# Kernel tuning notes

Hardware: AMD Instinct MI355X
Metric: run time of the kernel (lower is better)

Reference implementation:

```python
import jax, jax.numpy as jnp
import numpy as np
import math

EPS = 1e-5
GROUPS = 8


def setup_inputs() -> dict:
    key = jax.random.key(0)
    ks = jax.random.split(key, 4)
    b, c, h, w = 4, 256, 64, 64
    x = jax.random.normal(ks[0], (b, c, h, w), dtype=jnp.float32)
    norm_w = jnp.ones((c,), dtype=jnp.float32)
    norm_b = jnp.zeros((c,), dtype=jnp.float32)
    qkv_w = jax.random.normal(ks[1], (3 * c, c), dtype=jnp.float32) * (1.0 / math.sqrt(c))
    qkv_b = jnp.zeros((3 * c,), dtype=jnp.float32)
    proj_w = jax.random.normal(ks[2], (c, c), dtype=jnp.float32) * (1.0 / math.sqrt(c))
    proj_b = jnp.zeros((c,), dtype=jnp.float32)
    return {"x": x, "norm_w": norm_w, "norm_b": norm_b, "qkv_w": qkv_w,
            "qkv_b": qkv_b, "proj_w": proj_w, "proj_b": proj_b}


def group_norm(x, weight, bias):
    b, c, h, w = x.shape
    xg = x.reshape(b, GROUPS, c // GROUPS, h, w)
    mean = xg.mean(axis=(2, 3, 4), keepdims=True)
    var = xg.var(axis=(2, 3, 4), keepdims=True)
    xg = (xg - mean) * jax.lax.rsqrt(var + EPS)
    xn = xg.reshape(b, c, h, w)
    return xn * weight[None, :, None, None] + bias[None, :, None, None]


def reference(x, norm_w, norm_b, qkv_w, qkv_b, proj_w, proj_b):
    b, c, h, w = x.shape
    n = h * w
    xn = group_norm(x, norm_w, norm_b)
    # 1x1 conv == per-pixel linear: tokens [b, n, c]
    tokens = xn.reshape(b, c, n).transpose(0, 2, 1)
    qkv = jnp.einsum('bnc,oc->bno', tokens, qkv_w) + qkv_b  # [b, n, 3c]
    q, k, v = jnp.split(qkv, 3, axis=-1)
    scale = 1.0 / math.sqrt(c)
    attn = jnp.einsum('bqc,bkc->bqk', q, k) * scale  # [b, n, n]
    attn = jax.nn.softmax(attn, axis=-1)
    out = jnp.einsum('bqk,bkc->bqc', attn, v)  # [b, n, c]
    out = jnp.einsum('bnc,oc->bno', out, proj_w) + proj_b
    out = out.transpose(0, 2, 1).reshape(b, c, h, w)
    return x + out
```

## Files before the change

### kernel.cpp

```cpp
#include <hip/hip_runtime.h>
#include <math.h>

typedef unsigned short u16;
typedef __bf16 bf16x8 __attribute__((ext_vector_type(8)));
typedef u16    u16x8  __attribute__((ext_vector_type(8)));
typedef float  f32x4  __attribute__((ext_vector_type(4)));
typedef float  f32x16 __attribute__((ext_vector_type(16)));

__device__ __forceinline__ float b2f(u16 u) {
    union { unsigned u; float f; } x; x.u = ((unsigned)u) << 16; return x.f;
}
__device__ __forceinline__ u16 f2b(float f) {
    union { float f; unsigned u; } x; x.f = f;
    unsigned r = x.u + 0x7FFFu + ((x.u >> 16) & 1u);
    return (u16)(r >> 16);
}
__device__ __forceinline__ f32x4 mfma16(bf16x8 a, bf16x8 b, f32x4 c) {
    return __builtin_amdgcn_mfma_f32_16x16x32_bf16(a, b, c, 0, 0, 0);
}
__device__ __forceinline__ f32x16 mfma32(bf16x8 a, bf16x8 b, f32x16 c) {
    return __builtin_amdgcn_mfma_f32_32x32x16_bf16(a, b, c, 0, 0, 0);
}
__device__ __forceinline__ void dma16(const void* g, void* l) {
    __builtin_amdgcn_global_load_lds((const __attribute__((address_space(1))) void*)g,
                                     (__attribute__((address_space(3))) void*)l, 16, 0, 0);
}
__device__ __forceinline__ int dtype_vote(const unsigned* w) {
    unsigned v = w[threadIdx.x & 63];
    unsigned e = ((v & 0xFFFFu) >> 7) & 0xFFu;
    unsigned long long m = __ballot(e >= 0x60u && e <= 0x8Fu);
    return (__popcll(m) >= 32) ? 0 : 1;
}

#define QSCALE 0.09016844f

__global__ __launch_bounds__(256) void k_cvtx(const void* __restrict__ src, u16* __restrict__ dst,
                                              int* __restrict__ flag) {
    const int f = dtype_vote((const unsigned*)src);
    if (blockIdx.x == 0 && threadIdx.x == 0) *flag = f;
    const int i = (blockIdx.x * 256 + threadIdx.x) * 4;
    if (f) {
        float4 v = *(const float4*)((const float*)src + i);
        unsigned lo = (unsigned)f2b(v.x) | ((unsigned)f2b(v.y) << 16);
        unsigned hi = (unsigned)f2b(v.z) | ((unsigned)f2b(v.w) << 16);
        *(uint2*)(dst + i) = make_uint2(lo, hi);
    } else {
        *(uint2*)(dst + i) = *(const uint2*)((const u16*)src + i);
    }
}

__global__ __launch_bounds__(256) void k_cvtp(const void* s0, const void* s1, const void* s2,
                                              const void* s3, const void* s4, const void* s5,
                                              u16* d0, u16* d1, u16* d2, u16* d3, u16* d4, u16* d5) {
    const int f = dtype_vote((const unsigned*)s2);
    const int i = blockIdx.x * 256 + threadIdx.x;
    const void* s; u16* d; int j;
    if      (i < 256)    { s = s0; d = d0; j = i; }
    else if (i < 512)    { s = s1; d = d1; j = i - 256; }
    else if (i < 197120) { s = s2; d = d2; j = i - 512; }
    else if (i < 197888) { s = s3; d = d3; j = i - 197120; }
    else if (i < 263424) { s = s4; d = d4; j = i - 197888; }
    else if (i < 263680) { s = s5; d = d5; j = i - 263424; }
    else return;
    if (f) d[j] = f2b(((const float*)s)[j]);
    else   d[j] = ((const u16*)s)[j];
}

__global__ __launch_bounds__(256) void k_stats(const u16* __restrict__ x, float* __restrict__ stats) {
    const int bg = blockIdx.x;
    const u16* p = x + (size_t)bg * 131072;
    float s = 0.f, ss = 0.f;
    for (int i = threadIdx.x; i < 16384; i += 256) {
        bf16x8 v = *(const bf16x8*)(p + i * 8);
#pragma unroll
        for (int j = 0; j < 8; j++) { float f = (float)v[j]; s += f; ss += f * f; }
    }
#pragma unroll
    for (int o = 1; o < 64; o <<= 1) { s += __shfl_xor(s, o, 64); ss += __shfl_xor(ss, o, 64); }
    __shared__ float rs[4], rss[4];
    const int wv = threadIdx.x >> 6;
    if ((threadIdx.x & 63) == 0) { rs[wv] = s; rss[wv] = ss; }
    __syncthreads();
    if (threadIdx.x == 0) {
        s = rs[0] + rs[1] + rs[2] + rs[3];
        ss = rss[0] + rss[1] + rss[2] + rss[3];
        float mean = s * (1.f / 131072.f);
        float var = fmaxf(ss * (1.f / 131072.f) - mean * mean, 0.f);
        stats[bg] = mean;
        stats[32 + bg] = rsqrtf(var + 1e-5f);
    }
}

__global__ __launch_bounds__(256) void k_tok(const u16* __restrict__ x, const u16* __restrict__ nw,
                                             const u16* __restrict__ nb, const float* __restrict__ stats,
                                             u16* __restrict__ tok) {
    const int b = blockIdx.z, c0 = blockIdx.y * 64, p0 = blockIdx.x * 64;
    __shared__ u16 t[64][72];
    const int cl = threadIdx.x >> 2, seg = threadIdx.x & 3;
    const int c = c0 + cl;
    const int g = c >> 5;
    const float mean = stats[b * 8 + g], rstd = stats[32 + b * 8 + g];
    const float scale = b2f(nw[c]) * rstd;
    const float shift = b2f(nb[c]) - mean * scale;
    const u16* xp = x + ((size_t)(b * 256 + c)) * 4096 + p0 + seg * 16;
#pragma unroll
    for (int h = 0; h < 2; h++) {
        bf16x8 v = *(const bf16x8*)(xp + h * 8);
#pragma unroll
        for (int j = 0; j < 8; j++)
            t[seg * 16 + h * 8 + j][cl] = f2b((float)v[j] * scale + shift);
    }
    __syncthreads();
    u16x8 o0, o1;
#pragma unroll
    for (int j = 0; j < 8; j++) { o0[j] = t[cl][seg * 16 + j]; o1[j] = t[cl][seg * 16 + 8 + j]; }
    u16* op = tok + ((size_t)(b * 4096 + p0 + cl)) * 256 + c0 + seg * 16;
    *(u16x8*)op = o0;
    *((u16x8*)op + 1) = o1;
}

__global__ __launch_bounds__(256) void k_qkv(const u16* __restrict__ A, const u16* __restrict__ W,
                                             const u16* __restrict__ bias,
                                             u16* __restrict__ Qo, u16* __restrict__ Ko, u16* __restrict__ Vt) {
    const int m0 = blockIdx.x * 128, n0 = blockIdx.y * 128;
    const int tid = threadIdx.x, w = tid >> 6, lane = tid & 63, l15 = lane & 15, l4 = lane >> 4;
    const int wm = w >> 1, wn = w & 1;
    __shared__ __attribute__((aligned(16))) u16 At[128 * 64];
    __shared__ __attribute__((aligned(16))) u16 Bt[128 * 64];
    f32x4 acc[4][4];
    const f32x4 z = {0.f, 0.f, 0.f, 0.f};
#pragma unroll
    for (int i = 0; i < 4; i++)
#pragma unroll
        for (int j = 0; j < 4; j++) acc[i][j] = z;

    for (int kt = 0; kt < 4; kt++) {
        const int k0 = kt * 64;
#pragma unroll
        for (int i = 0; i < 4; i++) {
            int v = tid + i * 256;
            int row = v >> 3, c8 = v & 7;
            int swz = (c8 ^ (row & 7)) << 3;
            *(u16x8*)(&At[row * 64 + swz]) = *(const u16x8*)(A + (size_t)(m0 + row) * 256 + k0 + c8 * 8);
            *(u16x8*)(&Bt[row * 64 + swz]) = *(const u16x8*)(W + (size_t)(n0 + row) * 256 + k0 + c8 * 8);
        }
        __syncthreads();
#pragma unroll
        for (int ks = 0; ks < 2; ks++) {
            const int sc = ((ks * 4 + l4) ^ (l15 & 7)) << 3;
            bf16x8 af[4], bfr[4];
#pragma unroll
            for (int i = 0; i < 4; i++) {
                af[i]  = *(const bf16x8*)(&At[(wm * 64 + i * 16 + l15) * 64 + sc]);
                bfr[i] = *(const bf16x8*)(&Bt[(wn * 64 + i * 16 + l15) * 64 + sc]);
            }
#pragma unroll
            for (int i = 0; i < 4; i++)
#pragma unroll
                for (int j = 0; j < 4; j++) acc[i][j] = mfma16(af[i], bfr[j], acc[i][j]);
        }
        __syncthreads();
    }
#pragma unroll
    for (int j = 0; j < 4; j++) {
        const int n = n0 + wn * 64 + j * 16 + l15;
        const float bia = b2f(bias[n]);
#pragma unroll
        for (int i = 0; i < 4; i++) {
#pragma unroll
            for (int r = 0; r < 4; r++) {
                const int m = m0 + wm * 64 + i * 16 + l4 * 4 + r;
                const float vv = acc[i][j][r] + bia;
                if (n < 256)       Qo[(size_t)m * 256 + n] = f2b(vv * QSCALE);
                else if (n < 512)  Ko[(size_t)m * 256 + (n - 256)] = f2b(vv);
                else {
                    const int bb = m >> 12;
                    int p = m & 4095;
                    int d = ((p >> 2) ^ (p >> 3)) & 1;
                    p ^= d * 12;
                    Vt[((size_t)bb * 256 + (n - 512)) * 4096 + p] = f2b(vv);
                }
            }
        }
    }
}

__global__ __launch_bounds__(256, 2) void k_attn(const u16* __restrict__ Q, const u16* __restrict__ K,
                                                 const u16* __restrict__ Vt,
                                                 u16* __restrict__ Up, float* __restrict__ ml) {
    const int qt = blockIdx.x, b = blockIdx.y, sp = blockIdx.z;
    const int tid = threadIdx.x, w = tid >> 6, lane = tid & 63;
    const int l31 = lane & 31, h = lane >> 5;
    const int qcol = qt * 128 + w * 32 + l31;

    __shared__ __attribute__((aligned(16))) char LB[65536];
    u16* KT = (u16*)LB;
    u16* VT = (u16*)(LB + 32768);

    bf16x8 aq[16];
    {
        const u16* qp = Q + ((size_t)(b * 4096 + qcol)) * 256 + h * 8;
#pragma unroll
        for (int kb = 0; kb < 16; kb++) aq[kb] = *(const bf16x8*)(qp + kb * 16);
    }
    f32x16 acc[8];
#pragma unroll
    for (int ct = 0; ct < 8; ct++)
#pragma unroll
        for (int r = 0; r < 16; r++) acc[ct][r] = 0.f;
    float m_i = -3e38f, l_i = 0.f;

    const char* Kg0 = (const char*)(K + (size_t)(b * 4096 + sp * 1024) * 256);
    const char* Vg0 = (const char*)(Vt + (size_t)b * 256 * 4096 + sp * 1024);
    const int wb = (tid & 192) * 8;

#define ISSUE(bi, kt)                                                                        \
    {                                                                                        \
        const char* Kg = Kg0 + (size_t)(kt) * 32 * 512;                                      \
        const char* Vg = Vg0 + (size_t)(kt) * 64;                                            \
        _Pragma("unroll")                                                                    \
        for (int i = 0; i < 4; i++) {                                                        \
            int q = i * 256 + tid;                                                           \
            int row = q >> 5, c = q & 31;                                                    \
            dma16(Kg + row * 512 + ((c ^ row) << 4), &KT[(bi) * 8192 + (i * 256) * 8 + wb]); \
        }                                                                                    \
        _Pragma("unroll")                                                                    \
        for (int i = 0; i < 4; i++) {                                                        \
            int q = i * 256 + tid;                                                           \
            int row = q >> 2, c = q & 3;                                                     \
            dma16(Vg + (size_t)row * 8192 + ((c ^ ((row >> 3) & 3)) << 4),                   \
                  &VT[(bi) * 8192 + (i * 256) * 8 + wb]);                                    \
        }                                                                                    \
    }

    ISSUE(0, 0)
    ISSUE(1, 1)

    for (int kt = 0; kt < 32; kt++) {
        const int cur = kt & 1;
        if (kt < 31) asm volatile("s_waitcnt vmcnt(8)" ::: "memory");
        else         asm volatile("s_waitcnt vmcnt(0)" ::: "memory");
        asm volatile("s_barrier" ::: "memory");

        const u16* KTc = &KT[cur * 8192];
        const u16* VTc = &VT[cur * 8192];

        f32x16 st;
#pragma unroll
        for (int r = 0; r < 16; r++) st[r] = 0.f;
#pragma unroll
        for (int kb = 0; kb < 16; kb++) {
            bf16x8 bk = *(const bf16x8*)(&KTc[l31 * 256 + (((kb * 2 + h) ^ l31) << 3)]);
            st = mfma32(bk, aq[kb], st);
        }

        float mx = st[0];
#pragma unroll
        for (int r = 1; r < 16; r++) mx = fmaxf(mx, st[r]);
        mx = fmaxf(mx, __shfl_xor(mx, 32, 64));
        if (__any(mx > m_i + 4.f)) {
            const float m_new = fmaxf(m_i, mx);
            const float al = __builtin_amdgcn_exp2f(m_i - m_new);
#pragma unroll
            for (int ct = 0; ct < 8; ct++)
#pragma unroll
                for (int r = 0; r < 16; r++) acc[ct][r] *= al;
            l_i *= al;
            m_i = m_new;
        }
        float sum = 0.f;
#pragma unroll
        for (int r = 0; r < 16; r++) {
            st[r] = __builtin_amdgcn_exp2f(st[r] - m_i);
            sum += st[r];
        }
        sum += __shfl_xor(sum, 32, 64);
        l_i += sum;

        union { u16x8 u; bf16x8 bv; } p0, p1;
#pragma unroll
        for (int e = 0; e < 8; e++) { p0.u[e] = f2b(st[e]); p1.u[e] = f2b(st[8 + e]); }

#pragma unroll
        for (int ct = 0; ct < 8; ct++) {
            bf16x8 av0 = *(const bf16x8*)(&VTc[(ct * 32 + l31) * 32 + ((h ^ (l31 >> 3)) << 3)]);
            acc[ct] = mfma32(av0, p0.bv, acc[ct]);
            bf16x8 av1 = *(const bf16x8*)(&VTc[(ct * 32 + l31) * 32 + (((2 + h) ^ (l31 >> 3)) << 3)]);
            acc[ct] = mfma32(av1, p1.bv, acc[ct]);
        }
        asm volatile("s_barrier" ::: "memory");
        if (kt + 2 < 32) ISSUE(cur, kt + 2)
    }
#undef ISSUE

    if (h == 0)
        ((float2*)ml)[(size_t)(sp * 4 + b) * 4096 + qcol] = make_float2(m_i, l_i);
    u16* Ot = (u16*)(LB + w * 16384);
#pragma unroll
    for (int ct = 0; ct < 8; ct++) {
#pragma unroll
        for (int r = 0; r < 16; r++) {
            const int c = ct * 32 + (r & 3) + 8 * (r >> 2) + 4 * h;
            Ot[l31 * 256 + (((c >> 3) ^ l31) << 3) + (c & 7)] = f2b(acc[ct][r]);
        }
    }
    u16* up = Up + ((size_t)(sp * 4 + b) * 4096 + qt * 128 + w * 32) * 256;
#pragma unroll
    for (int v = 0; v < 16; v++) {
        int idx = v * 64 + lane;
        int qrow = idx >> 5, c8 = idx & 31;
        u16x8 d = *(const u16x8*)(&Ot[qrow * 256 + ((c8 ^ qrow) << 3)]);
        *(u16x8*)(up + (size_t)qrow * 256 + c8 * 8) = d;
    }
}

__global__ __launch_bounds__(256) void k_ml(const float* __restrict__ ml, float4* __restrict__ W4q) {
    const int t = blockIdx.x * 256 + threadIdx.x;
    const int b = t >> 12, q = t & 4095;
    float m_s[4], l_s[4];
#pragma unroll
    for (int s = 0; s < 4; s++) {
        float2 v = ((const float2*)ml)[(size_t)(s * 4 + b) * 4096 + q];
        m_s[s] = v.x; l_s[s] = v.y;
    }
    float M = fmaxf(fmaxf(m_s[0], m_s[1]), fmaxf(m_s[2], m_s[3]));
    float L = 0.f, e[4];
#pragma unroll
    for (int s = 0; s < 4; s++) { e[s] = __builtin_amdgcn_exp2f(m_s[s] - M); L += l_s[s] * e[s]; }
    float inv = 1.f / fmaxf(L, 1e-30f);
    W4q[t] = make_float4(e[0] * inv, e[1] * inv, e[2] * inv, e[3] * inv);
}

__global__ __launch_bounds__(256) void k_proj(const u16* __restrict__ Up, const float4* __restrict__ W4q,
                                              const u16* __restrict__ W, const u16* __restrict__ bias,
                                              const u16* __restrict__ x, void* __restrict__ out,
                                              const int* __restrict__ flag) {
    const int f32out = *flag;
    const int m0 = blockIdx.x * 64;
    const int b = m0 >> 12, q0 = m0 & 4095;
    const int tid = threadIdx.x, w = tid >> 6, lane = tid & 63, l15 = lane & 15, l4 = lane >> 4;
    const int wm = w >> 1, wn = w & 1;
    __shared__ __attribute__((aligned(16))) char PL[40960];
    u16* At = (u16*)PL;
    u16* Bt = (u16*)(PL + 8192);
    u16* Ot = (u16*)PL;

    const int qa = tid >> 2, ca = (tid & 3) * 16;
    const float4 wq = W4q[m0 + qa];
    const float wsv[4] = {wq.x, wq.y, wq.z, wq.w};
    const u16* upb = Up + (size_t)(q0 + qa) * 256 + ca;

    f32x4 acc[2][8];
    const f32x4 z = {0.f, 0.f, 0.f, 0.f};
#pragma unroll
    for (int i = 0; i < 2; i++)
#pragma unroll
        for (int j = 0; j < 8; j++) acc[i][j] = z;

    for (int kt = 0; kt < 4; kt++) {
        const int k0 = kt * 64;
        {
            float vs[16];
#pragma unroll
            for (int e = 0; e < 16; e++) vs[e] = 0.f;
#pragma unroll
            for (int s = 0; s < 4; s++) {
                const u16* p = upb + ((size_t)(s * 4 + b) * 4096) * 256 + k0;
                u16x8 u0 = *(const u16x8*)p;
                u16x8 u1 = *(const u16x8*)(p + 8);
                const float ws = wsv[s];
#pragma unroll
                for (int e = 0; e < 8; e++) { vs[e] += b2f(u0[e]) * ws; vs[8 + e] += b2f(u1[e]) * ws; }
            }
            u16x8 o0, o1;
#pragma unroll
            for (int e = 0; e < 8; e++) { o0[e] = f2b(vs[e]); o1[e] = f2b(vs[8 + e]); }
            const int c8 = ca >> 3;
            *(u16x8*)(&At[qa * 64 + ((c8 ^ (qa & 7)) << 3)]) = o0;
            *(u16x8*)(&At[qa * 64 + (((c8 + 1) ^ (qa & 7)) << 3)]) = o1;
        }
#pragma unroll
        for (int i = 0; i < 8; i++) {
            int v = i * 256 + tid;
            int row = v >> 3, c8 = v & 7;
            *(u16x8*)(&Bt[row * 64 + ((c8 ^ (row & 7)) << 3)]) =
                *(const u16x8*)(W + (size_t)row * 256 + k0 + c8 * 8);
        }
        __syncthreads();
#pragma unroll
        for (int ks = 0; ks < 2; ks++) {
            const int sc = ((ks * 4 + l4) ^ (l15 & 7)) << 3;
            bf16x8 af[2], bfr[8];
#pragma unroll
            for (int i = 0; i < 2; i++)
                af[i] = *(const bf16x8*)(&At[(wm * 32 + i * 16 + l15) * 64 + sc]);
#pragma unroll
            for (int j = 0; j < 8; j++)
                bfr[j] = *(const bf16x8*)(&Bt[(wn * 128 + j * 16 + l15) * 64 + sc]);
#pragma unroll
            for (int i = 0; i < 2; i++)
#pragma unroll
                for (int j = 0; j < 8; j++) acc[i][j] = mfma16(af[i], bfr[j], acc[i][j]);
        }
        __syncthreads();
    }

#pragma unroll
    for (int j = 0; j < 8; j++) {
        const int n = wn * 128 + j * 16 + l15;
        const float bia = b2f(bias[n]);
#pragma unroll
        for (int i = 0; i < 2; i++) {
#pragma unroll
            for (int r = 0; r < 4; r++) {
                const int p = wm * 32 + i * 16 + l4 * 4 + r;
                Ot[n * 64 + ((((p >> 3) ^ (n & 7)) << 3)) + (p & 7)] = f2b(acc[i][j][r] + bia);
            }
        }
    }
    __syncthreads();
    const int ps = (tid & 7) * 8;
#pragma unroll
    for (int v = 0; v < 8; v++) {
        const int n = v * 32 + (tid >> 3);
        u16x8 d = *(const u16x8*)(&Ot[n * 64 + ((((ps >> 3) ^ (n & 7)) << 3))]);
        const size_t base = ((size_t)(b * 256 + n)) * 4096 + q0 + ps;
        u16x8 xv = *(const u16x8*)(x + base);
        if (f32out) {
            float4 o0, o1;
#pragma unroll
            for (int e = 0; e < 4; e++) o0[e] = b2f(d[e]) + b2f(xv[e]);
#pragma unroll
            for (int e = 0; e < 4; e++) o1[e] = b2f(d[4 + e]) + b2f(xv[4 + e]);
            *(float4*)((float*)out + base) = o0;
            *(float4*)((float*)out + base + 4) = o1;
        } else {
            u16x8 o;
#pragma unroll
            for (int e = 0; e < 8; e++) o[e] = f2b(b2f(d[e]) + b2f(xv[e]));
            *(u16x8*)((u16*)out + base) = o;
        }
    }
}

extern "C" void kernel_launch(void* const* d_in, const int* in_sizes, int n_in,
                              void* d_out, int out_size, void* d_ws, size_t ws_size,
                              hipStream_t stream) {
    char* ws = (char*)d_ws;
    float* stats = (float*)ws;
    int*   flag  = (int*)(ws + 2048);
    u16* xb  = (u16*)(ws + 4096);
    u16* nwb = xb + (size_t)4194304;
    u16* nbb = nwb + 256;
    u16* qbb = nbb + 256;
    u16* pbb = qbb + 768;
    u16* pad = pbb + 256;
    u16* qwb = pad + 256;
    u16* pwb = qwb + (size_t)196608;
    u16* tok = pwb + (size_t)65536;
    u16* Qb  = tok + (size_t)16384 * 256;
    u16* Kb  = Qb  + (size_t)16384 * 256;
    u16* Vb  = Kb  + (size_t)16384 * 256;
    u16* Upb = Vb  + (size_t)16384 * 256;
    float* mlb = (float*)(Upb + (size_t)16 * 4096 * 256);
    float4* W4q = (float4*)(mlb + (size_t)16 * 4096 * 2);

    k_cvtx<<<dim3(4096), dim3(256), 0, stream>>>(d_in[0], xb, flag);
    k_cvtp<<<dim3(1030), dim3(256), 0, stream>>>(d_in[1], d_in[2], d_in[3], d_in[4], d_in[5], d_in[6],
                                                 nwb, nbb, qwb, qbb, pwb, pbb);

    k_stats<<<dim3(32), dim3(256), 0, stream>>>(xb, stats);
    k_tok  <<<dim3(64, 4, 4), dim3(256), 0, stream>>>(xb, nwb, nbb, stats, tok);
    k_qkv  <<<dim3(128, 6), dim3(256), 0, stream>>>(tok, qwb, qbb, Qb, Kb, Vb);
    k_attn <<<dim3(32, 4, 4), dim3(256), 0, stream>>>(Qb, Kb, Vb, Upb, mlb);
    k_ml   <<<dim3(64), dim3(256), 0, stream>>>(mlb, W4q);
    k_proj <<<dim3(256), dim3(256), 0, stream>>>(Upb, W4q, pwb, pbb, xb, d_out, flag);
}
```

Baseline: 238.8 us.

## Fuse group-norm stats into conversion, stage QKV stores, single-buffer attention

Group-norm partial sums are now computed inside the x conversion kernel and reduced by a tiny kernel, which removes a separate full pass over x. The QKV GEMM epilogue stages results in LDS with a swizzle and writes coalesced 16-byte rows for Q, K and the transposed V instead of scattered 2-byte stores. The softmax-merge kernel k_ml is folded into k_proj's prologue. The attention kernel drops its double-buffered async K/V prefetch for a single buffer with __syncthreads, which cuts LDS use but exposes load latency in the main loop.

```diff
diff --git a/kernel.cpp b/kernel.cpp
--- a/kernel.cpp
+++ b/kernel.cpp
@@ -35,17 +35,47 @@
 #define QSCALE 0.09016844f
 
 __global__ __launch_bounds__(256) void k_cvtx(const void* __restrict__ src, u16* __restrict__ dst,
-                                              int* __restrict__ flag) {
+                                              int* __restrict__ flag, float2* __restrict__ part) {
     const int f = dtype_vote((const unsigned*)src);
     if (blockIdx.x == 0 && threadIdx.x == 0) *flag = f;
     const int i = (blockIdx.x * 256 + threadIdx.x) * 4;
+    u16 o[4];
     if (f) {
         float4 v = *(const float4*)((const float*)src + i);
-        unsigned lo = (unsigned)f2b(v.x) | ((unsigned)f2b(v.y) << 16);
-        unsigned hi = (unsigned)f2b(v.z) | ((unsigned)f2b(v.w) << 16);
-        *(uint2*)(dst + i) = make_uint2(lo, hi);
+        o[0] = f2b(v.x); o[1] = f2b(v.y); o[2] = f2b(v.z); o[3] = f2b(v.w);
     } else {
-        *(uint2*)(dst + i) = *(const uint2*)((const u16*)src + i);
+        uint2 v = *(const uint2*)((const u16*)src + i);
+        o[0] = (u16)(v.x & 0xFFFF); o[1] = (u16)(v.x >> 16);
+        o[2] = (u16)(v.y & 0xFFFF); o[3] = (u16)(v.y >> 16);
+    }
+    unsigned lo = (unsigned)o[0] | ((unsigned)o[1] << 16);
+    unsigned hi = (unsigned)o[2] | ((unsigned)o[3] << 16);
+    *(uint2*)(dst + i) = make_uint2(lo, hi);
+    float s = 0.f, ss = 0.f;
+#pragma unroll
+    for (int e = 0; e < 4; e++) { float x = b2f(o[e]); s += x; ss += x * x; }
+#pragma unroll
+    for (int d = 1; d < 64; d <<= 1) { s += __shfl_xor(s, d, 64); ss += __shfl_xor(ss, d, 64); }
+    __shared__ float rs[4], rss[4];
+    const int wv = threadIdx.x >> 6;
+    if ((threadIdx.x & 63) == 0) { rs[wv] = s; rss[wv] = ss; }
+    __syncthreads();
+    if (threadIdx.x == 0)
+        part[blockIdx.x] = make_float2(rs[0] + rs[1] + rs[2] + rs[3],
+                                       rss[0] + rss[1] + rss[2] + rss[3]);
+}
+
+__global__ __launch_bounds__(64) void k_statsf(const float2* __restrict__ part, float* __restrict__ stats) {
+    const int g = blockIdx.x, lane = threadIdx.x;
+    float2 a = part[g * 128 + lane], b = part[g * 128 + 64 + lane];
+    float s = a.x + b.x, ss = a.y + b.y;
+#pragma unroll
+    for (int d = 1; d < 64; d <<= 1) { s += __shfl_xor(s, d, 64); ss += __shfl_xor(ss, d, 64); }
+    if (lane == 0) {
+        float mean = s * (1.f / 131072.f);
+        float var = fmaxf(ss * (1.f / 131072.f) - mean * mean, 0.f);
+        stats[g] = mean;
+        stats[32 + g] = rsqrtf(var + 1e-5f);
     }
 }
 
@@ -66,31 +96,6 @@
     else   d[j] = ((const u16*)s)[j];
 }
 
-__global__ __launch_bounds__(256) void k_stats(const u16* __restrict__ x, float* __restrict__ stats) {
-    const int bg = blockIdx.x;
-    const u16* p = x + (size_t)bg * 131072;
-    float s = 0.f, ss = 0.f;
-    for (int i = threadIdx.x; i < 16384; i += 256) {
-        bf16x8 v = *(const bf16x8*)(p + i * 8);
-#pragma unroll
-        for (int j = 0; j < 8; j++) { float f = (float)v[j]; s += f; ss += f * f; }
-    }
-#pragma unroll
-    for (int o = 1; o < 64; o <<= 1) { s += __shfl_xor(s, o, 64); ss += __shfl_xor(ss, o, 64); }
-    __shared__ float rs[4], rss[4];
-    const int wv = threadIdx.x >> 6;
-    if ((threadIdx.x & 63) == 0) { rs[wv] = s; rss[wv] = ss; }
-    __syncthreads();
-    if (threadIdx.x == 0) {
-        s = rs[0] + rs[1] + rs[2] + rs[3];
-        ss = rss[0] + rss[1] + rss[2] + rss[3];
-        float mean = s * (1.f / 131072.f);
-        float var = fmaxf(ss * (1.f / 131072.f) - mean * mean, 0.f);
-        stats[bg] = mean;
-        stats[32 + bg] = rsqrtf(var + 1e-5f);
-    }
-}
-
 __global__ __launch_bounds__(256) void k_tok(const u16* __restrict__ x, const u16* __restrict__ nw,
                                              const u16* __restrict__ nb, const float* __restrict__ stats,
                                              u16* __restrict__ tok) {
@@ -123,10 +128,14 @@
                                              const u16* __restrict__ bias,
                                              u16* __restrict__ Qo, u16* __restrict__ Ko, u16* __restrict__ Vt) {
     const int m0 = blockIdx.x * 128, n0 = blockIdx.y * 128;
+    const int cls = blockIdx.y >> 1, sub = (blockIdx.y & 1) * 128;
+    const int b = m0 >> 12, p0 = m0 & 4095;
     const int tid = threadIdx.x, w = tid >> 6, lane = tid & 63, l15 = lane & 15, l4 = lane >> 4;
     const int wm = w >> 1, wn = w & 1;
-    __shared__ __attribute__((aligned(16))) u16 At[128 * 64];
-    __shared__ __attribute__((aligned(16))) u16 Bt[128 * 64];
+    __shared__ __attribute__((aligned(16))) char QL[32768];
+    u16* At = (u16*)QL;
+    u16* Bt = (u16*)(QL + 16384);
+    u16* E  = (u16*)QL;
     f32x4 acc[4][4];
     const f32x4 z = {0.f, 0.f, 0.f, 0.f};
 #pragma unroll
@@ -161,26 +170,44 @@
         }
         __syncthreads();
     }
+
+    const float sf = (cls == 0) ? QSCALE : 1.f;
 #pragma unroll
     for (int j = 0; j < 4; j++) {
-        const int n = n0 + wn * 64 + j * 16 + l15;
-        const float bia = b2f(bias[n]);
+        const int nl = wn * 64 + j * 16 + l15;
+        const float bia = b2f(bias[n0 + nl]);
 #pragma unroll
         for (int i = 0; i < 4; i++) {
 #pragma unroll
             for (int r = 0; r < 4; r++) {
-                const int m = m0 + wm * 64 + i * 16 + l4 * 4 + r;
-                const float vv = acc[i][j][r] + bia;
-                if (n < 256)       Qo[(size_t)m * 256 + n] = f2b(vv * QSCALE);
-                else if (n < 512)  Ko[(size_t)m * 256 + (n - 256)] = f2b(vv);
-                else {
-                    const int bb = m >> 12;
-                    int p = m & 4095;
-                    int d = ((p >> 2) ^ (p >> 3)) & 1;
-                    p ^= d * 12;
-                    Vt[((size_t)bb * 256 + (n - 512)) * 4096 + p] = f2b(vv);
+                const int ml = wm * 64 + i * 16 + l4 * 4 + r;
+                const u16 val = f2b((acc[i][j][r] + bia) * sf);
+                if (cls < 2) {
+                    E[ml * 128 + (((nl >> 3) ^ (ml & 7)) << 3) + (nl & 7)] = val;
+                } else {
+                    int ps = ml ^ ((((ml >> 2) ^ (ml >> 3)) & 1) * 12);
+                    E[nl * 128 + (((ps >> 3) ^ (nl & 7)) << 3) + (ps & 7)] = val;
                 }
             }
+        }
+    }
+    __syncthreads();
+    const int row = tid >> 1, half = tid & 1;
+    if (cls < 2) {
+        u16* dst = (cls == 0 ? Qo : Ko) + (size_t)(m0 + row) * 256 + sub;
+#pragma unroll
+        for (int k = 0; k < 8; k++) {
+            const int chunk = half * 8 + k;
+            u16x8 v = *(const u16x8*)(&E[row * 128 + ((chunk ^ (row & 7)) << 3)]);
+            *(u16x8*)(dst + chunk * 8) = v;
+        }
+    } else {
+        u16* dst = Vt + (size_t)(b * 256 + sub + row) * 4096 + p0;
+#pragma unroll
+        for (int k = 0; k < 8; k++) {
+            const int chunk = half * 8 + k;
+            u16x8 v = *(const u16x8*)(&E[row * 128 + ((chunk ^ (row & 7)) << 3)]);
+            *(u16x8*)(dst + chunk * 8) = v;
         }
     }
 }
@@ -195,7 +222,7 @@
 
     __shared__ __attribute__((aligned(16))) char LB[65536];
     u16* KT = (u16*)LB;
-    u16* VT = (u16*)(LB + 32768);
+    u16* VT = (u16*)(LB + 16384);
 
     bf16x8 aq[16];
     {
@@ -210,47 +237,35 @@
         for (int r = 0; r < 16; r++) acc[ct][r] = 0.f;
     float m_i = -3e38f, l_i = 0.f;
 
-    const char* Kg0 = (const char*)(K + (size_t)(b * 4096 + sp * 1024) * 256);
-    const char* Vg0 = (const char*)(Vt + (size_t)b * 256 * 4096 + sp * 1024);
+    const u16* Kg0 = K + (size_t)(b * 4096 + sp * 1024) * 256;
+    const u16* Vg0 = Vt + (size_t)b * 256 * 4096 + sp * 1024;
     const int wb = (tid & 192) * 8;
 
-#define ISSUE(bi, kt)                                                                        \
-    {                                                                                        \
-        const char* Kg = Kg0 + (size_t)(kt) * 32 * 512;                                      \
-        const char* Vg = Vg0 + (size_t)(kt) * 64;                                            \
-        _Pragma("unroll")                                                                    \
-        for (int i = 0; i < 4; i++) {                                                        \
-            int q = i * 256 + tid;                                                           \
-            int row = q >> 5, c = q & 31;                                                    \
-            dma16(Kg + row * 512 + ((c ^ row) << 4), &KT[(bi) * 8192 + (i * 256) * 8 + wb]); \
-        }                                                                                    \
-        _Pragma("unroll")                                                                    \
-        for (int i = 0; i < 4; i++) {                                                        \
-            int q = i * 256 + tid;                                                           \
-            int row = q >> 2, c = q & 3;                                                     \
-            dma16(Vg + (size_t)row * 8192 + ((c ^ ((row >> 3) & 3)) << 4),                   \
-                  &VT[(bi) * 8192 + (i * 256) * 8 + wb]);                                    \
-        }                                                                                    \
-    }
-
-    ISSUE(0, 0)
-    ISSUE(1, 1)
-
     for (int kt = 0; kt < 32; kt++) {
-        const int cur = kt & 1;
-        if (kt < 31) asm volatile("s_waitcnt vmcnt(8)" ::: "memory");
-        else         asm volatile("s_waitcnt vmcnt(0)" ::: "memory");
-        asm volatile("s_barrier" ::: "memory");
-
-        const u16* KTc = &KT[cur * 8192];
-        const u16* VTc = &VT[cur * 8192];
+        {
+            const u16* Kg = Kg0 + (size_t)kt * 32 * 256;
+#pragma unroll
+            for (int i = 0; i < 4; i++) {
+                int q = i * 256 + tid;
+                int row = q >> 5, c = q & 31;
+                dma16(Kg + row * 256 + ((c ^ row) << 3), &KT[i * 2048 + wb]);
+            }
+            const u16* Vg = Vg0 + kt * 32;
+#pragma unroll
+            for (int i = 0; i < 4; i++) {
+                int q = i * 256 + tid;
+                int row = q >> 2, c = q & 3;
+                dma16(Vg + (size_t)row * 4096 + ((c ^ ((row >> 3) & 3)) << 3), &VT[i * 2048 + wb]);
+            }
+        }
+        __syncthreads();
 
         f32x16 st;
 #pragma unroll
         for (int r = 0; r < 16; r++) st[r] = 0.f;
 #pragma unroll
         for (int kb = 0; kb < 16; kb++) {
-            bf16x8 bk = *(const bf16x8*)(&KTc[l31 * 256 + (((kb * 2 + h) ^ l31) << 3)]);
+            bf16x8 bk = *(const bf16x8*)(&KT[l31 * 256 + (((kb * 2 + h) ^ l31) << 3)]);
             st = mfma32(bk, aq[kb], st);
         }
 
@@ -283,15 +298,13 @@
 
 #pragma unroll
         for (int ct = 0; ct < 8; ct++) {
-            bf16x8 av0 = *(const bf16x8*)(&VTc[(ct * 32 + l31) * 32 + ((h ^ (l31 >> 3)) << 3)]);
+            bf16x8 av0 = *(const bf16x8*)(&VT[(ct * 32 + l31) * 32 + ((h ^ (l31 >> 3)) << 3)]);
             acc[ct] = mfma32(av0, p0.bv, acc[ct]);
-            bf16x8 av1 = *(const bf16x8*)(&VTc[(ct * 32 + l31) * 32 + (((2 + h) ^ (l31 >> 3)) << 3)]);
+            bf16x8 av1 = *(const bf16x8*)(&VT[(ct * 32 + l31) * 32 + (((2 + h) ^ (l31 >> 3)) << 3)]);
             acc[ct] = mfma32(av1, p1.bv, acc[ct]);
         }
-        asm volatile("s_barrier" ::: "memory");
-        if (kt + 2 < 32) ISSUE(cur, kt + 2)
-    }
-#undef ISSUE
+        __syncthreads();
+    }
 
     if (h == 0)
         ((float2*)ml)[(size_t)(sp * 4 + b) * 4096 + qcol] = make_float2(m_i, l_i);
@@ -314,24 +327,7 @@
     }
 }
 
-__global__ __launch_bounds__(256) void k_ml(const float* __restrict__ ml, float4* __restrict__ W4q) {
-    const int t = blockIdx.x * 256 + threadIdx.x;
-    const int b = t >> 12, q = t & 4095;
-    float m_s[4], l_s[4];
-#pragma unroll
-    for (int s = 0; s < 4; s++) {
-        float2 v = ((const float2*)ml)[(size_t)(s * 4 + b) * 4096 + q];
-        m_s[s] = v.x; l_s[s] = v.y;
-    }
-    float M = fmaxf(fmaxf(m_s[0], m_s[1]), fmaxf(m_s[2], m_s[3]));
-    float L = 0.f, e[4];
-#pragma unroll
-    for (int s = 0; s < 4; s++) { e[s] = __builtin_amdgcn_exp2f(m_s[s] - M); L += l_s[s] * e[s]; }
-    float inv = 1.f / fmaxf(L, 1e-30f);
-    W4q[t] = make_float4(e[0] * inv, e[1] * inv, e[2] * inv, e[3] * inv);
-}
-
-__global__ __launch_bounds__(256) void k_proj(const u16* __restrict__ Up, const float4* __restrict__ W4q,
+__global__ __launch_bounds__(256) void k_proj(const u16* __restrict__ Up, const float* __restrict__ ml,
                                               const u16* __restrict__ W, const u16* __restrict__ bias,
                                               const u16* __restrict__ x, void* __restrict__ out,
                                               const int* __restrict__ flag) {
@@ -344,9 +340,27 @@
     u16* At = (u16*)PL;
     u16* Bt = (u16*)(PL + 8192);
     u16* Ot = (u16*)PL;
+    __shared__ float4 W4s[64];
+
+    if (tid < 64) {
+        const int q = q0 + tid;
+        float m_s[4], l_s[4];
+#pragma unroll
+        for (int s = 0; s < 4; s++) {
+            float2 v = ((const float2*)ml)[(size_t)(s * 4 + b) * 4096 + q];
+            m_s[s] = v.x; l_s[s] = v.y;
+        }
+        float M = fmaxf(fmaxf(m_s[0], m_s[1]), fmaxf(m_s[2], m_s[3]));
+        float L = 0.f, e[4];
+#pragma unroll
+        for (int s = 0; s < 4; s++) { e[s] = __builtin_amdgcn_exp2f(m_s[s] - M); L += l_s[s] * e[s]; }
+        float inv = 1.f / fmaxf(L, 1e-30f);
+        W4s[tid] = make_float4(e[0] * inv, e[1] * inv, e[2] * inv, e[3] * inv);
+    }
+    __syncthreads();
 
     const int qa = tid >> 2, ca = (tid & 3) * 16;
-    const float4 wq = W4q[m0 + qa];
+    const float4 wq = W4s[qa];
     const float wsv[4] = {wq.x, wq.y, wq.z, wq.w};
     const u16* upb = Up + (size_t)(q0 + qa) * 256 + ca;
 
@@ -449,7 +463,8 @@
     char* ws = (char*)d_ws;
     float* stats = (float*)ws;
     int*   flag  = (int*)(ws + 2048);
-    u16* xb  = (u16*)(ws + 4096);
+    float2* part = (float2*)(ws + 4096);
+    u16* xb  = (u16*)(ws + 65536);
     u16* nwb = xb + (size_t)4194304;
     u16* nbb = nwb + 256;
     u16* qbb = nbb + 256;
@@ -463,16 +478,14 @@
     u16* Vb  = Kb  + (size_t)16384 * 256;
     u16* Upb = Vb  + (size_t)16384 * 256;
     float* mlb = (float*)(Upb + (size_t)16 * 4096 * 256);
-    float4* W4q = (float4*)(mlb + (size_t)16 * 4096 * 2);
-
-    k_cvtx<<<dim3(4096), dim3(256), 0, stream>>>(d_in[0], xb, flag);
-    k_cvtp<<<dim3(1030), dim3(256), 0, stream>>>(d_in[1], d_in[2], d_in[3], d_in[4], d_in[5], d_in[6],
-                                                 nwb, nbb, qwb, qbb, pwb, pbb);
-
-    k_stats<<<dim3(32), dim3(256), 0, stream>>>(xb, stats);
-    k_tok  <<<dim3(64, 4, 4), dim3(256), 0, stream>>>(xb, nwb, nbb, stats, tok);
-    k_qkv  <<<dim3(128, 6), dim3(256), 0, stream>>>(tok, qwb, qbb, Qb, Kb, Vb);
-    k_attn <<<dim3(32, 4, 4), dim3(256), 0, stream>>>(Qb, Kb, Vb, Upb, mlb);
-    k_ml   <<<dim3(64), dim3(256), 0, stream>>>(mlb, W4q);
-    k_proj <<<dim3(256), dim3(256), 0, stream>>>(Upb, W4q, pwb, pbb, xb, d_out, flag);
-}
+
+    k_cvtx  <<<dim3(4096), dim3(256), 0, stream>>>(d_in[0], xb, flag, part);
+    k_statsf<<<dim3(32), dim3(64), 0, stream>>>(part, stats);
+    k_cvtp  <<<dim3(1030), dim3(256), 0, stream>>>(d_in[1], d_in[2], d_in[3], d_in[4], d_in[5], d_in[6],
+                                                   nwb, nbb, qwb, qbb, pwb, pbb);
+
+    k_tok <<<dim3(64, 4, 4), dim3(256), 0, stream>>>(xb, nwb, nbb, stats, tok);
+    k_qkv <<<dim3(128, 6), dim3(256), 0, stream>>>(tok, qwb, qbb, Qb, Kb, Vb);
+    k_attn<<<dim3(32, 4, 4), dim3(256), 0, stream>>>(Qb, Kb, Vb, Upb, mlb);
+    k_proj<<<dim3(256), dim3(256), 0, stream>>>(Upb, mlb, pwb, pbb, xb, d_out, flag);
+}
```

After: 223.4 us. -6.5%, faster.
